# Performance work log

Measured on AMD Instinct MI355X. Metric: run time of the kernel, lower is better.

## Reference

```python
import jax, jax.numpy as jnp
import numpy as np

B, IN, U = 8192, 64, 128
UNFOLDS = 3
EPS = 1e-8


def setup_inputs() -> dict:
    key = jax.random.key(0)
    ks = jax.random.split(key, 12)
    inputs = jax.random.normal(ks[0], (B, IN), dtype=jnp.float32)
    state = jax.random.normal(ks[1], (B, U), dtype=jnp.float32)
    sensory_mu = jax.random.uniform(ks[2], (IN, U), minval=0.4, maxval=0.6)
    sensory_sigma = jax.random.uniform(ks[3], (IN, U), minval=1.0, maxval=2.0)
    sensory_W = jax.random.uniform(ks[4], (IN, U), minval=0.01, maxval=1.0)
    sensory_erev = (2.0 * jax.random.randint(ks[5], (IN, U), 0, 2) - 1.0).astype(jnp.float32)
    mu = jax.random.uniform(ks[6], (U, U), minval=0.4, maxval=0.6)
    sigma = jax.random.uniform(ks[7], (U, U), minval=1.0, maxval=2.0)
    W = jax.random.uniform(ks[8], (U, U), minval=0.01, maxval=1.0)
    erev = (2.0 * jax.random.randint(ks[9], (U, U), 0, 2) - 1.0).astype(jnp.float32)
    vleak = jax.random.uniform(ks[10], (U,), minval=-0.2, maxval=0.2)
    gleak = jnp.ones((U,), dtype=jnp.float32)
    cm_t = jnp.full((U,), 0.5, dtype=jnp.float32)
    return {"inputs": inputs, "state": state,
            "sensory_mu": sensory_mu, "sensory_sigma": sensory_sigma,
            "sensory_W": sensory_W, "sensory_erev": sensory_erev,
            "mu": mu, "sigma": sigma, "W": W, "erev": erev,
            "vleak": vleak, "gleak": gleak, "cm_t": cm_t}


def _gate(v_pre, mu, sigma):
    # v_pre: [B, F] -> [B, F, 1]; mu, sigma: [F, U]
    x = sigma * (v_pre[:, :, None] - mu)
    return jax.nn.sigmoid(x)  # [B, F, U]


def reference(inputs, state, sensory_mu, sensory_sigma, sensory_W, sensory_erev,
              mu, sigma, W, erev, vleak, gleak, cm_t):
    # sensory conductances (computed once)
    sensory_w_act = sensory_W * _gate(inputs, sensory_mu, sensory_sigma)  # [B, IN, U]
    w_num_sensory = jnp.sum(sensory_w_act * sensory_erev, axis=1)         # [B, U]
    w_den_sensory = jnp.sum(sensory_w_act, axis=1)                        # [B, U]

    v_pre = state
    for _ in range(UNFOLDS):
        w_act = W * _gate(v_pre, mu, sigma)                # [B, U, U]
        w_num = jnp.sum(w_act * erev, axis=1) + w_num_sensory
        w_den = jnp.sum(w_act, axis=1) + w_den_sensory
        numerator = cm_t * v_pre + gleak * vleak + w_num
        denominator = cm_t + gleak + w_den
        v_pre = numerator / (denominator + EPS)
    return v_pre
```

## Files before the change

kernel.cpp:

```cpp
#include <hip/hip_runtime.h>
#include <hip/hip_fp16.h>
#include <cstdint>

namespace {

typedef _Float16 h2 __attribute__((ext_vector_type(2)));

constexpr int BATCH   = 8192;
constexpr int IN      = 64;
constexpr int U       = 128;
constexpr int R       = 4;
constexpr int TB      = 32;
constexpr int NT      = 1024;
constexpr int UNFOLDS = 3;
constexpr int PAD     = 36;
constexpr float LOG2E = 1.4426950408889634f;

union HU { uint32_t u; h2 h; };

__device__ __forceinline__ uint32_t pack2(float lo, float hi) {
  __half l = __float2half_rn(lo);
  __half h = __float2half_rn(hi);
  return (uint32_t)__half_as_ushort(l) | ((uint32_t)__half_as_ushort(h) << 16);
}

__device__ __forceinline__ void gate2(float A0, float B0, float A1, float B1,
                                      h2 wpk, h2 wepk, float v0, float v1,
                                      float& num, float& den) {
  const float t0 = fmaf(A0, v0, B0);
  const float t1 = fmaf(A1, v1, B1);
  const float e0 = __builtin_amdgcn_exp2f(t0);
  const float e1 = __builtin_amdgcn_exp2f(t1);
  const float a0 = 1.0f + e0;
  const float a1 = 1.0f + e1;
  const float r  = __builtin_amdgcn_rcpf(a0 * a1);
  const float rc0 = a1 * r;
  const float rc1 = a0 * r;
  const h2 rpk = __builtin_bit_cast(h2, __builtin_amdgcn_cvt_pkrtz(rc0, rc1));
  den = __builtin_amdgcn_fdot2(rpk, wpk,  den, false);
  num = __builtin_amdgcn_fdot2(rpk, wepk, num, false);
}

__global__ __launch_bounds__(NT, 4)
void ltc_fused(const float* __restrict__ inputs, const float* __restrict__ state,
               const float* __restrict__ s_mu, const float* __restrict__ s_sigma,
               const float* __restrict__ s_W, const float* __restrict__ s_erev,
               const float* __restrict__ r_mu, const float* __restrict__ r_sigma,
               const float* __restrict__ r_W, const float* __restrict__ r_erev,
               const float* __restrict__ vleak, const float* __restrict__ gleak,
               const float* __restrict__ cm_t, float* __restrict__ out)
{
  __shared__ uint4 pack_s[(U / 2) * U];
  __shared__ float vp_s[U][PAD];
  __shared__ float inp_s[IN][PAD];

  const int tid = threadIdx.x;
  const int u   = tid & (U - 1);
  const int bl  = tid >> 7;
  const int b0  = blockIdx.x * TB;

  const float cm   = cm_t[u];
  const float gl   = gleak[u];
  const float numc = gl * vleak[u];
  const float denc = cm + gl + 1e-8f;

  for (int k = tid; k < (IN / 2) * U; k += NT) {
    const int p  = k >> 7;
    const int uu = k & (U - 1);
    const int i0 = 2 * p, i1 = i0 + 1;
    const float sg0 = s_sigma[i0 * U + uu], sg1 = s_sigma[i1 * U + uu];
    const float w0  = s_W[i0 * U + uu],     w1  = s_W[i1 * U + uu];
    uint4 q;
    q.x = pack2(-LOG2E * sg0, LOG2E * sg0 * s_mu[i0 * U + uu]);
    q.y = pack2(-LOG2E * sg1, LOG2E * sg1 * s_mu[i1 * U + uu]);
    q.z = pack2(w0, w1);
    q.w = pack2(w0 * s_erev[i0 * U + uu], w1 * s_erev[i1 * U + uu]);
    pack_s[k] = q;
  }
  for (int k = tid; k < TB * IN; k += NT) {
    const int bloc = k >> 6;
    const int i    = k & (IN - 1);
    inp_s[i][bloc] = inputs[b0 * IN + k];
  }
  for (int k = tid; k < TB * U; k += NT) {
    const int bloc = k >> 7;
    const int i    = k & (U - 1);
    vp_s[i][bloc] = state[b0 * U + k];
  }
  float vo[R];
#pragma unroll
  for (int r = 0; r < R; ++r) vo[r] = state[(b0 + bl * R + r) * U + u];
  __syncthreads();

  float num_s[R], den_s[R];
#pragma unroll
  for (int r = 0; r < R; ++r) { num_s[r] = 0.f; den_s[r] = 0.f; }
#pragma unroll 4
  for (int p = 0; p < IN / 2; ++p) {
    const uint4 q = pack_s[p * U + u];
    const float4 va = *reinterpret_cast<const float4*>(&inp_s[2 * p][bl * R]);
    const float4 vb = *reinterpret_cast<const float4*>(&inp_s[2 * p + 1][bl * R]);
    HU x, y, z, w; x.u = q.x; y.u = q.y; z.u = q.z; w.u = q.w;
    const float A0 = (float)x.h.x, B0 = (float)x.h.y;
    const float A1 = (float)y.h.x, B1 = (float)y.h.y;
#pragma unroll
    for (int r = 0; r < R; ++r)
      gate2(A0, B0, A1, B1, z.h, w.h, (&va.x)[r], (&vb.x)[r], num_s[r], den_s[r]);
  }
  __syncthreads();

  for (int k = tid; k < (U / 2) * U; k += NT) {
    const int p  = k >> 7;
    const int uu = k & (U - 1);
    const int i0 = 2 * p, i1 = i0 + 1;
    const float sg0 = r_sigma[i0 * U + uu], sg1 = r_sigma[i1 * U + uu];
    const float w0  = r_W[i0 * U + uu],     w1  = r_W[i1 * U + uu];
    uint4 q;
    q.x = pack2(-LOG2E * sg0, LOG2E * sg0 * r_mu[i0 * U + uu]);
    q.y = pack2(-LOG2E * sg1, LOG2E * sg1 * r_mu[i1 * U + uu]);
    q.z = pack2(w0, w1);
    q.w = pack2(w0 * r_erev[i0 * U + uu], w1 * r_erev[i1 * U + uu]);
    pack_s[k] = q;
  }
  __syncthreads();

#pragma unroll
  for (int t = 0; t < UNFOLDS; ++t) {
    float num[R], den[R];
#pragma unroll
    for (int r = 0; r < R; ++r) { num[r] = num_s[r]; den[r] = den_s[r]; }
#pragma unroll 4
    for (int p = 0; p < U / 2; ++p) {
      const uint4 q = pack_s[p * U + u];
      const float4 va = *reinterpret_cast<const float4*>(&vp_s[2 * p][bl * R]);
      const float4 vb = *reinterpret_cast<const float4*>(&vp_s[2 * p + 1][bl * R]);
      HU x, y, z, w; x.u = q.x; y.u = q.y; z.u = q.z; w.u = q.w;
      const float A0 = (float)x.h.x, B0 = (float)x.h.y;
      const float A1 = (float)y.h.x, B1 = (float)y.h.y;
#pragma unroll
      for (int r = 0; r < R; ++r)
        gate2(A0, B0, A1, B1, z.h, w.h, (&va.x)[r], (&vb.x)[r], num[r], den[r]);
    }
    float vnew[R];
#pragma unroll
    for (int r = 0; r < R; ++r) {
      vnew[r] = (fmaf(cm, vo[r], numc) + num[r]) * __builtin_amdgcn_rcpf(denc + den[r]);
      vo[r] = vnew[r];
    }
    if (t == UNFOLDS - 1) {
#pragma unroll
      for (int r = 0; r < R; ++r) out[(b0 + bl * R + r) * U + u] = vnew[r];
    } else {
      __syncthreads();
      *reinterpret_cast<float4*>(&vp_s[u][bl * R]) =
          make_float4(vnew[0], vnew[1], vnew[2], vnew[3]);
      __syncthreads();
    }
  }
}

}

extern "C" void kernel_launch(void* const* d_in, const int* in_sizes, int n_in,
                              void* d_out, int out_size, void* d_ws, size_t ws_size,
                              hipStream_t stream) {
  const float* inputs   = (const float*)d_in[0];
  const float* state    = (const float*)d_in[1];
  const float* s_mu     = (const float*)d_in[2];
  const float* s_sigma  = (const float*)d_in[3];
  const float* s_W      = (const float*)d_in[4];
  const float* s_erev   = (const float*)d_in[5];
  const float* r_mu     = (const float*)d_in[6];
  const float* r_sigma  = (const float*)d_in[7];
  const float* r_W      = (const float*)d_in[8];
  const float* r_erev   = (const float*)d_in[9];
  const float* vleak    = (const float*)d_in[10];
  const float* gleak    = (const float*)d_in[11];
  const float* cm_t     = (const float*)d_in[12];
  float* out = (float*)d_out;

  ltc_fused<<<dim3(BATCH / TB), dim3(NT), 0, stream>>>(
      inputs, state, s_mu, s_sigma, s_W, s_erev,
      r_mu, r_sigma, r_W, r_erev, vleak, gleak, cm_t, out);
}
```

Before: 108.7 us.

## Prepack gate parameters in a separate kernel and read them from global memory

Adds a prepack kernel that converts the sensory and recurrent mu/sigma/W/erev parameters once into packed fp16 quads in the workspace. The main kernel now reads those quads straight from global/L2 instead of rebuilding them in shared memory in every block, which removes the per-block packing work and the large shared buffer. It also halves the block to 512 threads and 16 batch rows with an occupancy hint of 8, aiming at more resident blocks. In exchange, every inner-loop iteration issues an uncached-by-LDS global load, and there is an extra kernel launch. The old fused kernel stays as a fallback when the workspace is too small.

```diff
diff --git a/kernel.cpp b/kernel.cpp
--- a/kernel.cpp
+++ b/kernel.cpp
@@ -10,11 +10,18 @@
 constexpr int IN      = 64;
 constexpr int U       = 128;
 constexpr int R       = 4;
-constexpr int TB      = 32;
-constexpr int NT      = 1024;
 constexpr int UNFOLDS = 3;
-constexpr int PAD     = 36;
 constexpr float LOG2E = 1.4426950408889634f;
+
+constexpr int NT   = 512;
+constexpr int TB   = 16;
+constexpr int PADV = 20;
+constexpr int SENP = (IN / 2) * U;
+constexpr int RECP = (U / 2) * U;
+
+constexpr int FNT  = 1024;
+constexpr int FTB  = 32;
+constexpr int FPAD = 36;
 
 union HU { uint32_t u; h2 h; };
 
@@ -41,7 +48,126 @@
   num = __builtin_amdgcn_fdot2(rpk, wepk, num, false);
 }
 
-__global__ __launch_bounds__(NT, 4)
+__global__ __launch_bounds__(256)
+void prepack(const float* __restrict__ s_mu, const float* __restrict__ s_sigma,
+             const float* __restrict__ s_W, const float* __restrict__ s_erev,
+             const float* __restrict__ r_mu, const float* __restrict__ r_sigma,
+             const float* __restrict__ r_W, const float* __restrict__ r_erev,
+             uint4* __restrict__ pw)
+{
+  const int k = blockIdx.x * 256 + threadIdx.x;
+  if (k < SENP) {
+    const int p = k >> 7, uu = k & (U - 1);
+    const int i0 = 2 * p, i1 = i0 + 1;
+    const float sg0 = s_sigma[i0 * U + uu], sg1 = s_sigma[i1 * U + uu];
+    const float w0  = s_W[i0 * U + uu],     w1  = s_W[i1 * U + uu];
+    uint4 q;
+    q.x = pack2(-LOG2E * sg0, LOG2E * sg0 * s_mu[i0 * U + uu]);
+    q.y = pack2(-LOG2E * sg1, LOG2E * sg1 * s_mu[i1 * U + uu]);
+    q.z = pack2(w0, w1);
+    q.w = pack2(w0 * s_erev[i0 * U + uu], w1 * s_erev[i1 * U + uu]);
+    pw[k] = q;
+  } else if (k < SENP + RECP) {
+    const int kk = k - SENP;
+    const int p = kk >> 7, uu = kk & (U - 1);
+    const int i0 = 2 * p, i1 = i0 + 1;
+    const float sg0 = r_sigma[i0 * U + uu], sg1 = r_sigma[i1 * U + uu];
+    const float w0  = r_W[i0 * U + uu],     w1  = r_W[i1 * U + uu];
+    uint4 q;
+    q.x = pack2(-LOG2E * sg0, LOG2E * sg0 * r_mu[i0 * U + uu]);
+    q.y = pack2(-LOG2E * sg1, LOG2E * sg1 * r_mu[i1 * U + uu]);
+    q.z = pack2(w0, w1);
+    q.w = pack2(w0 * r_erev[i0 * U + uu], w1 * r_erev[i1 * U + uu]);
+    pw[k] = q;
+  }
+}
+
+__global__ __launch_bounds__(NT, 8)
+void ltc_main(const uint4* __restrict__ pw,
+              const float* __restrict__ inputs, const float* __restrict__ state,
+              const float* __restrict__ vleak, const float* __restrict__ gleak,
+              const float* __restrict__ cm_t, float* __restrict__ out)
+{
+  __shared__ float vp_s[U][PADV];
+  __shared__ float inp_s[IN][PADV];
+
+  const int tid = threadIdx.x;
+  const int u   = tid & (U - 1);
+  const int bl  = tid >> 7;
+  const int b0  = blockIdx.x * TB;
+
+  const float cm   = cm_t[u];
+  const float gl   = gleak[u];
+  const float numc = gl * vleak[u];
+  const float denc = cm + gl + 1e-8f;
+
+  for (int k = tid; k < TB * IN; k += NT) {
+    const int bloc = k >> 6;
+    const int i    = k & (IN - 1);
+    inp_s[i][bloc] = inputs[b0 * IN + k];
+  }
+  for (int k = tid; k < TB * U; k += NT) {
+    const int bloc = k >> 7;
+    const int i    = k & (U - 1);
+    vp_s[i][bloc] = state[b0 * U + k];
+  }
+  float vo[R];
+#pragma unroll
+  for (int r = 0; r < R; ++r) vo[r] = state[(b0 + bl * R + r) * U + u];
+  __syncthreads();
+
+  float num_s[R], den_s[R];
+#pragma unroll
+  for (int r = 0; r < R; ++r) { num_s[r] = 0.f; den_s[r] = 0.f; }
+#pragma unroll 2
+  for (int p = 0; p < IN / 2; ++p) {
+    const uint4 q = pw[p * U + u];
+    const float4 va = *reinterpret_cast<const float4*>(&inp_s[2 * p][bl * R]);
+    const float4 vb = *reinterpret_cast<const float4*>(&inp_s[2 * p + 1][bl * R]);
+    HU x, y, z, w; x.u = q.x; y.u = q.y; z.u = q.z; w.u = q.w;
+    const float A0 = (float)x.h.x, B0 = (float)x.h.y;
+    const float A1 = (float)y.h.x, B1 = (float)y.h.y;
+#pragma unroll
+    for (int r = 0; r < R; ++r)
+      gate2(A0, B0, A1, B1, z.h, w.h, (&va.x)[r], (&vb.x)[r], num_s[r], den_s[r]);
+  }
+
+#pragma unroll
+  for (int t = 0; t < UNFOLDS; ++t) {
+    float num[R], den[R];
+#pragma unroll
+    for (int r = 0; r < R; ++r) { num[r] = num_s[r]; den[r] = den_s[r]; }
+#pragma unroll 2
+    for (int p = 0; p < U / 2; ++p) {
+      const uint4 q = pw[SENP + p * U + u];
+      const float4 va = *reinterpret_cast<const float4*>(&vp_s[2 * p][bl * R]);
+      const float4 vb = *reinterpret_cast<const float4*>(&vp_s[2 * p + 1][bl * R]);
+      HU x, y, z, w; x.u = q.x; y.u = q.y; z.u = q.z; w.u = q.w;
+      const float A0 = (float)x.h.x, B0 = (float)x.h.y;
+      const float A1 = (float)y.h.x, B1 = (float)y.h.y;
+#pragma unroll
+      for (int r = 0; r < R; ++r)
+        gate2(A0, B0, A1, B1, z.h, w.h, (&va.x)[r], (&vb.x)[r], num[r], den[r]);
+    }
+    float vnew[R];
+#pragma unroll
+    for (int r = 0; r < R; ++r) {
+      vnew[r] = (fmaf(cm, vo[r], numc) + num[r]) * __builtin_amdgcn_rcpf(denc + den[r]);
+      vo[r] = vnew[r];
+    }
+    if (t == UNFOLDS - 1) {
+#pragma unroll
+      for (int r = 0; r < R; ++r) out[(b0 + bl * R + r) * U + u] = vnew[r];
+    } else {
+      __syncthreads();
+      *reinterpret_cast<float4*>(&vp_s[u][bl * R]) =
+          make_float4(vnew[0], vnew[1], vnew[2], vnew[3]);
+      __syncthreads();
+    }
+  }
+}
+
+__global__ __launch_bounds__(FNT, 4)
 void ltc_fused(const float* __restrict__ inputs, const float* __restrict__ state,
                const float* __restrict__ s_mu, const float* __restrict__ s_sigma,
                const float* __restrict__ s_W, const float* __restrict__ s_erev,
@@ -51,20 +177,20 @@
                const float* __restrict__ cm_t, float* __restrict__ out)
 {
   __shared__ uint4 pack_s[(U / 2) * U];
-  __shared__ float vp_s[U][PAD];
-  __shared__ float inp_s[IN][PAD];
+  __shared__ float vp_s[U][FPAD];
+  __shared__ float inp_s[IN][FPAD];
 
   const int tid = threadIdx.x;
   const int u   = tid & (U - 1);
   const int bl  = tid >> 7;
-  const int b0  = blockIdx.x * TB;
+  const int b0  = blockIdx.x * FTB;
 
   const float cm   = cm_t[u];
   const float gl   = gleak[u];
   const float numc = gl * vleak[u];
   const float denc = cm + gl + 1e-8f;
 
-  for (int k = tid; k < (IN / 2) * U; k += NT) {
+  for (int k = tid; k < (IN / 2) * U; k += FNT) {
     const int p  = k >> 7;
     const int uu = k & (U - 1);
     const int i0 = 2 * p, i1 = i0 + 1;
@@ -77,15 +203,11 @@
     q.w = pack2(w0 * s_erev[i0 * U + uu], w1 * s_erev[i1 * U + uu]);
     pack_s[k] = q;
   }
-  for (int k = tid; k < TB * IN; k += NT) {
-    const int bloc = k >> 6;
-    const int i    = k & (IN - 1);
-    inp_s[i][bloc] = inputs[b0 * IN + k];
-  }
-  for (int k = tid; k < TB * U; k += NT) {
-    const int bloc = k >> 7;
-    const int i    = k & (U - 1);
-    vp_s[i][bloc] = state[b0 * U + k];
+  for (int k = tid; k < FTB * IN; k += FNT) {
+    inp_s[k & (IN - 1)][k >> 6] = inputs[b0 * IN + k];
+  }
+  for (int k = tid; k < FTB * U; k += FNT) {
+    vp_s[k & (U - 1)][k >> 7] = state[b0 * U + k];
   }
   float vo[R];
 #pragma unroll
@@ -109,7 +231,7 @@
   }
   __syncthreads();
 
-  for (int k = tid; k < (U / 2) * U; k += NT) {
+  for (int k = tid; k < (U / 2) * U; k += FNT) {
     const int p  = k >> 7;
     const int uu = k & (U - 1);
     const int i0 = 2 * p, i1 = i0 + 1;
@@ -179,7 +301,16 @@
   const float* cm_t     = (const float*)d_in[12];
   float* out = (float*)d_out;
 
-  ltc_fused<<<dim3(BATCH / TB), dim3(NT), 0, stream>>>(
-      inputs, state, s_mu, s_sigma, s_W, s_erev,
-      r_mu, r_sigma, r_W, r_erev, vleak, gleak, cm_t, out);
-}
+  const size_t need = (size_t)(SENP + RECP) * sizeof(uint4);
+  if (ws_size >= need) {
+    uint4* pw = (uint4*)d_ws;
+    prepack<<<dim3((SENP + RECP + 255) / 256), dim3(256), 0, stream>>>(
+        s_mu, s_sigma, s_W, s_erev, r_mu, r_sigma, r_W, r_erev, pw);
+    ltc_main<<<dim3(BATCH / TB), dim3(NT), 0, stream>>>(
+        pw, inputs, state, vleak, gleak, cm_t, out);
+  } else {
+    ltc_fused<<<dim3(BATCH / FTB), dim3(FNT), 0, stream>>>(
+        inputs, state, s_mu, s_sigma, s_W, s_erev,
+        r_mu, r_sigma, r_W, r_erev, vleak, gleak, cm_t, out);
+  }
+}
```

After: 117.4 us. 8.0% more time.
